# Kernel optimization log

Measured on AMD Instinct MI355X. Metric: run time of the kernel, lower is better.

Reference implementation:

```python
import jax, jax.numpy as jnp
import numpy as np

BIG = 1e30  # finite stand-in for +inf to keep grads clean


def _chamfer_loss(bin_center, ground_truth):
    # bin_center: [B, n_bins, 1] 1-D 'point cloud' of bin centers
    # ground_truth: [B, 1, H, W] depth map
    B = bin_center.shape[0]
    c = bin_center[..., 0]                      # [B, nb]
    p = ground_truth.reshape(B, -1)             # [B, V] flattened depth points
    mask = p >= 0.001                           # valid (non-near-zero) depths
    n = jnp.sum(mask, axis=1)                   # [B] valid count per sample
    Lmax = jnp.max(n)                           # pad_sequence pads every sample to L_max
    npad = (Lmax - n).astype(c.dtype)           # number of zero pad-points per sample

    # pairwise squared distances between bin centers and depth points
    D = (c[:, :, None] - p[:, None, :]) ** 2    # [B, nb, V]

    # direction 1: gt points -> nearest bin center (sum over points)
    dmin_p = jnp.min(D, axis=1)                 # [B, V]
    sumA = jnp.sum(jnp.where(mask, dmin_p, 0.0), axis=1)
    # each zero pad-point contributes min_j c_j^2
    c2 = c ** 2                                 # [B, nb]
    sumA = sumA + npad * jnp.min(c2, axis=1)

    # direction 2: bin centers -> nearest gt point (incl. zero pad-points if any)
    Dm = jnp.where(mask[:, None, :], D, jnp.asarray(BIG, D.dtype))
    min_valid = jnp.min(Dm, axis=2)             # [B, nb] min over valid points
    has_pad = (npad > 0)[:, None]
    min_b = jnp.where(has_pad, jnp.minimum(min_valid, c2), min_valid)
    sumB = jnp.sum(min_b, axis=1)               # [B]

    # chamferdist: point_reduction=sum, batch_reduction=mean, bidirectional
    return jnp.mean(sumA + sumB)


def setup_inputs() -> dict:
    key = jax.random.key(0)
    k1, k2 = jax.random.split(key)
    bin_center = jax.random.uniform(k1, (4, 256, 1), dtype=jnp.float32)
    ground_truth = jax.random.uniform(k2, (4, 1, 352, 448), dtype=jnp.float32)
    return {"bin_center": bin_center, "ground_truth": ground_truth}


def reference(bin_center, ground_truth):
    return _chamfer_loss(bin_center, ground_truth)
```

## Files before the change

### kernel.cpp

```cpp
#include <hip/hip_runtime.h>

#define NB   256
#define TPB  256
#define NI   (NB + 1)
#define G    128
#define P    5
#define MINF 1e30f
#define CAPD 1e15f

__global__ __launch_bounds__(NB) void k_sort(const float* __restrict__ bc,
                                             float* __restrict__ sbins,
                                             unsigned* __restrict__ gmin,
                                             unsigned* __restrict__ gmax) {
    __shared__ float s[NB];
    const int tid = threadIdx.x, b = blockIdx.x;
    s[tid] = bc[b * NB + tid];
    for (int t = tid; t < NI; t += NB) {
        gmin[b * NI + t] = 0xFFFFFFFFu;
        gmax[b * NI + t] = 0u;
    }
    __syncthreads();
    for (int k = 2; k <= NB; k <<= 1)
        for (int j = k >> 1; j > 0; j >>= 1) {
            const int ixj = tid ^ j;
            if (ixj > tid) {
                const float a = s[tid], bv = s[ixj];
                if ((a > bv) == ((tid & k) == 0)) { s[tid] = bv; s[ixj] = a; }
            }
            __syncthreads();
        }
    sbins[b * NB + tid] = s[tid];
}

__global__ __launch_bounds__(TPB) void k_main(
    const float* __restrict__ sbins, const float* __restrict__ gt,
    int V, int CH,
    float* __restrict__ sumA_part, int* __restrict__ cnt_part,
    unsigned* __restrict__ gmin, unsigned* __restrict__ gmax)
{
    const int b   = blockIdx.x / G;
    const int blk = blockIdx.x % G;
    const int tid = threadIdx.x;
    const int start = blk * CH;
    const int cn = min(CH, V - start);
    const float* __restrict__ gp = gt + (size_t)b * V + start;

    __shared__ float    c[NB];
    __shared__ unsigned imn[NI], imx[NI];
    c[tid] = sbins[b * NB + tid];
    for (int t = tid; t < NI; t += TPB) { imn[t] = 0xFFFFFFFFu; imx[t] = 0u; }
    __syncthreads();

    float q[P];
    #pragma unroll
    for (int p = 0; p < P; ++p) {
        const int i = tid + p * TPB;
        q[p] = (i < cn) ? gp[i] : -1.f;
    }

    int idx[P];
    #pragma unroll
    for (int p = 0; p < P; ++p) idx[p] = 0;
    #pragma unroll
    for (int st = 128; st >= 1; st >>= 1) {
        #pragma unroll
        for (int p = 0; p < P; ++p)
            idx[p] += (c[idx[p] + st - 1] <= q[p]) ? st : 0;
    }
    #pragma unroll
    for (int p = 0; p < P; ++p)
        idx[p] += (c[idx[p]] <= q[p]) ? 1 : 0;

    float sum = 0.f; int cnt = 0;
    #pragma unroll
    for (int p = 0; p < P; ++p) {
        if (q[p] >= 0.001f) {
            const float dlo = (idx[p] > 0)  ? (q[p] - c[idx[p] - 1]) : MINF;
            const float dhi = (idx[p] < NB) ? (c[idx[p]] - q[p])     : MINF;
            const float d = fminf(dlo, dhi);
            sum += d * d; ++cnt;
            atomicMin(&imn[idx[p]], __float_as_uint(q[p]));
            atomicMax(&imx[idx[p]], __float_as_uint(q[p]));
        }
    }
    __syncthreads();

    for (int t = tid; t < NI; t += TPB) {
        const unsigned lo = imn[t], hi = imx[t];
        if (lo != 0xFFFFFFFFu) atomicMin(&gmin[b * NI + t], lo);
        if (hi != 0u)          atomicMax(&gmax[b * NI + t], hi);
    }

    for (int off = 32; off; off >>= 1) {
        sum += __shfl_down(sum, off);
        cnt += __shfl_down(cnt, off);
    }
    __shared__ float r4[4]; __shared__ int i4[4];
    if ((tid & 63) == 0) { r4[tid >> 6] = sum; i4[tid >> 6] = cnt; }
    __syncthreads();
    if (tid == 0) {
        sumA_part[blockIdx.x] = r4[0] + r4[1] + r4[2] + r4[3];
        cnt_part [blockIdx.x] = i4[0] + i4[1] + i4[2] + i4[3];
    }
}

__global__ __launch_bounds__(TPB) void k_final(
    const float* __restrict__ sbins,
    const float* __restrict__ sumA_part, const int* __restrict__ cnt_part,
    const unsigned* __restrict__ gmin, const unsigned* __restrict__ gmax,
    int B, float* __restrict__ out)
{
    const int tid = threadIdx.x;
    __shared__ float pm[NB], sm[NB];
    __shared__ float r4[4]; __shared__ int i4[4]; __shared__ float q4[4];
    __shared__ float ssa[8]; __shared__ int sn[8];

    for (int bb = 0; bb < B; ++bb) {
        float s = 0.f; int cc = 0;
        for (int k = tid; k < G; k += TPB) {
            s  += sumA_part[bb * G + k];
            cc += cnt_part [bb * G + k];
        }
        for (int off = 32; off; off >>= 1) { s += __shfl_down(s, off); cc += __shfl_down(cc, off); }
        if ((tid & 63) == 0) { r4[tid >> 6] = s; i4[tid >> 6] = cc; }
        __syncthreads();
        if (tid == 0) { ssa[bb] = r4[0]+r4[1]+r4[2]+r4[3]; sn[bb] = i4[0]+i4[1]+i4[2]+i4[3]; }
        __syncthreads();
    }
    int Lmax = 0;
    for (int bb = 0; bb < B; ++bb) Lmax = max(Lmax, sn[bb]);

    float total = 0.f;
    for (int bb = 0; bb < B; ++bb) {
        const unsigned hib = gmax[bb * NI + tid];
        const unsigned lob = gmin[bb * NI + tid + 1];
        pm[tid] = (hib == 0u)          ? -MINF : __uint_as_float(hib);
        sm[tid] = (lob == 0xFFFFFFFFu) ?  MINF : __uint_as_float(lob);
        __syncthreads();
        for (int off = 1; off < NB; off <<= 1) {
            const float vp = pm[tid], vs = sm[tid];
            const float op = (tid >= off)     ? pm[tid - off] : -MINF;
            const float os = (tid + off < NB) ? sm[tid + off] :  MINF;
            __syncthreads();
            pm[tid] = fmaxf(vp, op);
            sm[tid] = fminf(vs, os);
            __syncthreads();
        }
        const float cj = sbins[bb * NB + tid];
        const float c2 = cj * cj;
        const float d  = fminf(fminf(cj - pm[tid], sm[tid] - cj), CAPD);
        float bm = d * d;
        const int npad = Lmax - sn[bb];
        if (npad > 0) bm = fminf(bm, c2);
        float s = bm, mc = c2;
        for (int off = 32; off; off >>= 1) {
            s  += __shfl_down(s, off);
            mc  = fminf(mc, __shfl_down(mc, off));
        }
        if ((tid & 63) == 0) { r4[tid >> 6] = s; q4[tid >> 6] = mc; }
        __syncthreads();
        if (tid == 0)
            total += ssa[bb]
                   + (float)npad * fminf(fminf(q4[0], q4[1]), fminf(q4[2], q4[3]))
                   + (r4[0] + r4[1] + r4[2] + r4[3]);
        __syncthreads();
    }
    if (tid == 0) out[0] = total / (float)B;
}

extern "C" void kernel_launch(void* const* d_in, const int* in_sizes, int n_in,
                              void* d_out, int out_size, void* d_ws, size_t ws_size,
                              hipStream_t stream) {
    const float* bc = (const float*)d_in[0];
    const float* gt = (const float*)d_in[1];
    const int B  = in_sizes[0] / NB;
    const int V  = in_sizes[1] / B;
    const int CH = (V + G - 1) / G;

    float*    sbins     = (float*)d_ws;
    float*    sumA_part = sbins + (size_t)B * NB;
    int*      cnt_part  = (int*)(sumA_part + (size_t)B * G);
    unsigned* gmin      = (unsigned*)(cnt_part + (size_t)B * G);
    unsigned* gmax      = gmin + (size_t)B * NI;

    k_sort <<<B, NB, 0, stream>>>(bc, sbins, gmin, gmax);
    k_main <<<B * G, TPB, 0, stream>>>(sbins, gt, V, CH,
                                       sumA_part, cnt_part, gmin, gmax);
    k_final<<<1, TPB, 0, stream>>>(sbins, sumA_part, cnt_part,
                                   gmin, gmax, B, (float*)d_out);
}
```

Before: 77.86 us.

## Fuse bin sort into main kernel and replace global atomics with per-block distances

```diff
diff --git a/kernel.cpp b/kernel.cpp
--- a/kernel.cpp
+++ b/kernel.cpp
@@ -8,48 +8,39 @@
 #define MINF 1e30f
 #define CAPD 1e15f
 
-__global__ __launch_bounds__(NB) void k_sort(const float* __restrict__ bc,
-                                             float* __restrict__ sbins,
-                                             unsigned* __restrict__ gmin,
-                                             unsigned* __restrict__ gmax) {
-    __shared__ float s[NB];
-    const int tid = threadIdx.x, b = blockIdx.x;
-    s[tid] = bc[b * NB + tid];
-    for (int t = tid; t < NI; t += NB) {
-        gmin[b * NI + t] = 0xFFFFFFFFu;
-        gmax[b * NI + t] = 0u;
-    }
-    __syncthreads();
-    for (int k = 2; k <= NB; k <<= 1)
-        for (int j = k >> 1; j > 0; j >>= 1) {
-            const int ixj = tid ^ j;
-            if (ixj > tid) {
-                const float a = s[tid], bv = s[ixj];
-                if ((a > bv) == ((tid & k) == 0)) { s[tid] = bv; s[ixj] = a; }
-            }
-            __syncthreads();
-        }
-    sbins[b * NB + tid] = s[tid];
-}
-
 __global__ __launch_bounds__(TPB) void k_main(
-    const float* __restrict__ sbins, const float* __restrict__ gt,
+    const float* __restrict__ bc, const float* __restrict__ gt,
     int V, int CH,
     float* __restrict__ sumA_part, int* __restrict__ cnt_part,
-    unsigned* __restrict__ gmin, unsigned* __restrict__ gmax)
+    float* __restrict__ bdist, float* __restrict__ sbins)
 {
-    const int b   = blockIdx.x / G;
-    const int blk = blockIdx.x % G;
-    const int tid = threadIdx.x;
+    const int b    = blockIdx.x / G;
+    const int blk  = blockIdx.x % G;
+    const int tid  = threadIdx.x;
+    const int lane = tid & 63, w = tid >> 6;
+
+    __shared__ float    raw[NB], c[NB];
+    __shared__ unsigned imn[NI], imx[NI];
+    __shared__ float wtop[4], wbot[4];
+    __shared__ float r4[4]; __shared__ int i4[4];
+
+    const float v = bc[b * NB + tid];
+    raw[tid] = v;
+    for (int t = tid; t < NI; t += TPB) { imn[t] = 0xFFFFFFFFu; imx[t] = 0u; }
+    __syncthreads();
+    int rank = 0;
+    #pragma unroll 16
+    for (int j = 0; j < NB; ++j) {
+        const float rj = raw[j];
+        rank += (rj < v || (rj == v && j < tid)) ? 1 : 0;
+    }
+    c[rank] = v;
+    __syncthreads();
+    if (blk == 0) sbins[b * NB + tid] = c[tid];
+
     const int start = blk * CH;
     const int cn = min(CH, V - start);
     const float* __restrict__ gp = gt + (size_t)b * V + start;
-
-    __shared__ float    c[NB];
-    __shared__ unsigned imn[NI], imx[NI];
-    c[tid] = sbins[b * NB + tid];
-    for (int t = tid; t < NI; t += TPB) { imn[t] = 0xFFFFFFFFu; imx[t] = 0u; }
-    __syncthreads();
 
     float q[P];
     #pragma unroll
@@ -85,18 +76,39 @@
     }
     __syncthreads();
 
-    for (int t = tid; t < NI; t += TPB) {
-        const unsigned lo = imn[t], hi = imx[t];
-        if (lo != 0xFFFFFFFFu) atomicMin(&gmin[b * NI + t], lo);
-        if (hi != 0u)          atomicMax(&gmax[b * NI + t], hi);
+    {
+        const unsigned hib = imx[tid];
+        const unsigned lob = imn[tid + 1];
+        float pv = (hib == 0u)          ? -MINF : __uint_as_float(hib);
+        float sv = (lob == 0xFFFFFFFFu) ?  MINF : __uint_as_float(lob);
+        #pragma unroll
+        for (int off = 1; off < 64; off <<= 1) {
+            const float o = __shfl_up(pv, off);
+            if (lane >= off) pv = fmaxf(pv, o);
+        }
+        #pragma unroll
+        for (int off = 1; off < 64; off <<= 1) {
+            const float o = __shfl_down(sv, off);
+            if (lane < 64 - off) sv = fminf(sv, o);
+        }
+        if (lane == 63) wtop[w] = pv;
+        if (lane == 0)  wbot[w] = sv;
+        __syncthreads();
+        #pragma unroll
+        for (int ww = 0; ww < 4; ++ww) {
+            if (ww < w) pv = fmaxf(pv, wtop[ww]);
+            if (ww > w) sv = fminf(sv, wbot[ww]);
+        }
+        const float cj = c[tid];
+        const float db = fminf(fminf(cj - pv, sv - cj), CAPD);
+        bdist[(size_t)blockIdx.x * NB + tid] = db;
     }
 
     for (int off = 32; off; off >>= 1) {
         sum += __shfl_down(sum, off);
         cnt += __shfl_down(cnt, off);
     }
-    __shared__ float r4[4]; __shared__ int i4[4];
-    if ((tid & 63) == 0) { r4[tid >> 6] = sum; i4[tid >> 6] = cnt; }
+    if (lane == 0) { r4[w] = sum; i4[w] = cnt; }
     __syncthreads();
     if (tid == 0) {
         sumA_part[blockIdx.x] = r4[0] + r4[1] + r4[2] + r4[3];
@@ -107,11 +119,10 @@
 __global__ __launch_bounds__(TPB) void k_final(
     const float* __restrict__ sbins,
     const float* __restrict__ sumA_part, const int* __restrict__ cnt_part,
-    const unsigned* __restrict__ gmin, const unsigned* __restrict__ gmax,
+    const float* __restrict__ bdist,
     int B, float* __restrict__ out)
 {
     const int tid = threadIdx.x;
-    __shared__ float pm[NB], sm[NB];
     __shared__ float r4[4]; __shared__ int i4[4]; __shared__ float q4[4];
     __shared__ float ssa[8]; __shared__ int sn[8];
 
@@ -132,24 +143,14 @@
 
     float total = 0.f;
     for (int bb = 0; bb < B; ++bb) {
-        const unsigned hib = gmax[bb * NI + tid];
-        const unsigned lob = gmin[bb * NI + tid + 1];
-        pm[tid] = (hib == 0u)          ? -MINF : __uint_as_float(hib);
-        sm[tid] = (lob == 0xFFFFFFFFu) ?  MINF : __uint_as_float(lob);
-        __syncthreads();
-        for (int off = 1; off < NB; off <<= 1) {
-            const float vp = pm[tid], vs = sm[tid];
-            const float op = (tid >= off)     ? pm[tid - off] : -MINF;
-            const float os = (tid + off < NB) ? sm[tid + off] :  MINF;
-            __syncthreads();
-            pm[tid] = fmaxf(vp, op);
-            sm[tid] = fminf(vs, os);
-            __syncthreads();
-        }
+        const float* __restrict__ bd = bdist + (size_t)(bb * G) * NB + tid;
+        float dm = bd[0];
+        #pragma unroll 8
+        for (int k = 1; k < G; ++k) dm = fminf(dm, bd[(size_t)k * NB]);
+
         const float cj = sbins[bb * NB + tid];
         const float c2 = cj * cj;
-        const float d  = fminf(fminf(cj - pm[tid], sm[tid] - cj), CAPD);
-        float bm = d * d;
+        float bm = dm * dm;
         const int npad = Lmax - sn[bb];
         if (npad > 0) bm = fminf(bm, c2);
         float s = bm, mc = c2;
@@ -177,15 +178,13 @@
     const int V  = in_sizes[1] / B;
     const int CH = (V + G - 1) / G;
 
-    float*    sbins     = (float*)d_ws;
-    float*    sumA_part = sbins + (size_t)B * NB;
-    int*      cnt_part  = (int*)(sumA_part + (size_t)B * G);
-    unsigned* gmin      = (unsigned*)(cnt_part + (size_t)B * G);
-    unsigned* gmax      = gmin + (size_t)B * NI;
+    float* sbins     = (float*)d_ws;
+    float* sumA_part = sbins + (size_t)B * NB;
+    int*   cnt_part  = (int*)(sumA_part + (size_t)B * G);
+    float* bdist     = (float*)(cnt_part + (size_t)B * G);
 
-    k_sort <<<B, NB, 0, stream>>>(bc, sbins, gmin, gmax);
-    k_main <<<B * G, TPB, 0, stream>>>(sbins, gt, V, CH,
-                                       sumA_part, cnt_part, gmin, gmax);
+    k_main <<<B * G, TPB, 0, stream>>>(bc, gt, V, CH,
+                                       sumA_part, cnt_part, bdist, sbins);
     k_final<<<1, TPB, 0, stream>>>(sbins, sumA_part, cnt_part,
-                                   gmin, gmax, B, (float*)d_out);
+                                   bdist, B, (float*)d_out);
 }
```

Measured after the change: 153.7 us. +97.4%, slower.
